# Optimization experiments

Measured on AMD Instinct MI355X. Metric: run time of the kernel, lower is better.

Reference implementation:

```python
import jax, jax.numpy as jnp
import numpy as np

N_NODES = 200000
N_EDGES = 440000
N_GRAPHS = 4096
EMB = 300
N_LAYERS = 5
TEMP = 0.04
NUM_ATOM_TYPE, NUM_CHIRALITY = 120, 3
NUM_BOND_TYPE, NUM_BOND_DIR = 6, 3
SELF_LOOP_TYPE = 4  # pretrain-gnns convention: self-loop edge_attr = [4, 0]


def setup_inputs() -> dict:
    key = jax.random.key(0)
    ks = jax.random.split(key, 24)
    inp = {}
    for i in (0, 1):
        inp[f"x{i}"] = jax.random.randint(ks[i * 4 + 0], (N_NODES, 2), 0, 3)
        inp[f"edge_index{i}"] = jax.random.randint(ks[i * 4 + 1], (2, N_EDGES), 0, N_NODES)
        inp[f"edge_attr{i}"] = jax.random.randint(ks[i * 4 + 2], (N_EDGES, 2), 0, 3)
        inp[f"batch_ids{i}"] = jnp.sort(jax.random.randint(ks[i * 4 + 3], (N_NODES,), 0, N_GRAPHS))

    def rn(k, shape, s=0.1):
        return (jax.random.normal(k, shape, jnp.float32) * s)

    inp["atom_emb1"] = rn(ks[8], (NUM_ATOM_TYPE, EMB))
    inp["atom_emb2"] = rn(ks[9], (NUM_CHIRALITY, EMB))
    inp["edge_emb1"] = rn(ks[10], (N_LAYERS, NUM_BOND_TYPE, EMB))
    inp["edge_emb2"] = rn(ks[11], (N_LAYERS, NUM_BOND_DIR, EMB))
    inp["W1"] = rn(ks[12], (N_LAYERS, EMB, 2 * EMB))
    inp["bm1"] = jnp.zeros((N_LAYERS, 2 * EMB), jnp.float32)
    inp["W2"] = rn(ks[13], (N_LAYERS, 2 * EMB, EMB))
    inp["bm2"] = jnp.zeros((N_LAYERS, EMB), jnp.float32)
    inp["gamma"] = jnp.ones((N_LAYERS, EMB), jnp.float32)
    inp["beta"] = jnp.zeros((N_LAYERS, EMB), jnp.float32)
    inp["Wp1"] = rn(ks[14], (EMB, EMB))
    inp["bp1"] = jnp.zeros((EMB,), jnp.float32)
    inp["Wp2"] = rn(ks[15], (EMB, EMB))
    inp["bp2"] = jnp.zeros((EMB,), jnp.float32)
    return inp


def _encode(x, edge_index, edge_attr, batch_ids,
            atom_emb1, atom_emb2, edge_emb1, edge_emb2,
            W1, bm1, W2, bm2, gamma, beta, Wp1, bp1, Wp2, bp2):
    n = x.shape[0]
    src, dst = edge_index[0], edge_index[1]
    h = atom_emb1[x[:, 0]] + atom_emb2[x[:, 1]]  # [N, EMB]
    for l in range(N_LAYERS):
        e = edge_emb1[l][edge_attr[:, 0]] + edge_emb2[l][edge_attr[:, 1]]  # [E, EMB]
        self_e = edge_emb1[l][SELF_LOOP_TYPE] + edge_emb2[l][0]  # self-loop edge emb
        # GIN sum aggregation (incl. self-loop message h_i + self_e)
        agg = jax.ops.segment_sum(h[src] + e, dst, num_segments=n) + h + self_e
        h = jax.nn.relu(agg @ W1[l] + bm1[l]) @ W2[l] + bm2[l]
        # BatchNorm over nodes (training-mode statistics, eps=1e-5)
        mean = h.mean(axis=0)
        var = h.var(axis=0)
        h = (h - mean) * jax.lax.rsqrt(var + 1e-5) * gamma[l] + beta[l]
        if l < N_LAYERS - 1:
            h = jax.nn.relu(h)
    # global_mean_pool
    s = jax.ops.segment_sum(h, batch_ids, num_segments=N_GRAPHS)
    c = jax.ops.segment_sum(jnp.ones((n, 1), h.dtype), batch_ids, num_segments=N_GRAPHS)
    g = s / jnp.maximum(c, 1.0)
    out = jax.nn.relu(g @ Wp1 + bp1) @ Wp2 + bp2
    return out / jnp.linalg.norm(out, axis=1, keepdims=True)


def reference(x0, edge_index0, edge_attr0, batch_ids0,
              x1, edge_index1, edge_attr1, batch_ids1,
              atom_emb1, atom_emb2, edge_emb1, edge_emb2,
              W1, bm1, W2, bm2, gamma, beta, Wp1, bp1, Wp2, bp2):
    params = (atom_emb1, atom_emb2, edge_emb1, edge_emb2,
              W1, bm1, W2, bm2, gamma, beta, Wp1, bp1, Wp2, bp2)
    f0 = _encode(x0, edge_index0, edge_attr0, batch_ids0, *params)
    f1 = _encode(x1, edge_index1, edge_attr1, batch_ids1, *params)
    logits = (f0 @ f1.T) / TEMP
    labels = jnp.arange(logits.shape[0])
    return logits, labels
```

## Files before the change

kernel.cpp:

```cpp
#include <hip/hip_runtime.h>
#include <hip/hip_bf16.h>
#include <hip/hip_fp16.h>

#define EMB 300
#define NHID 600
#define NLAYERS 5
#define NG 4096
#define NCOMBO 18
#define SELFCB 12
#define HS 304
#define KP1 320
#define KP2 640
#define SCB 2048

__device__ __forceinline__ void atomAddF(float* p, float v) { unsafeAtomicAdd(p, v); }

struct f8 { unsigned char v; };

__device__ __forceinline__ unsigned char enc8(float x) {
    unsigned xb = __float_as_uint(x);
    unsigned s = (xb >> 24) & 0x80u;
    float a = __uint_as_float(xb & 0x7FFFFFFFu);
    if (!(a < 448.f)) return (unsigned char)(s | 0x7E);
    if (a < 0.0009765625f) return (unsigned char)s;
    if (a < 0.015625f) {
        int m = (int)(a * 512.f + 0.5f);
        if (m > 7) return (unsigned char)(s | 0x08);
        return (unsigned char)(s | (unsigned)m);
    }
    unsigned u = __float_as_uint(a) + 0x80000u;
    int e = (int)(u >> 23) - 127;
    if (e > 8) return (unsigned char)(s | 0x7E);
    unsigned m = (u >> 20) & 7u;
    return (unsigned char)(s | ((unsigned)(e + 7) << 3) | m);
}
__device__ __forceinline__ float dec8(unsigned char c) {
    unsigned s = c & 0x80u, e = (c >> 3) & 0xFu, m = c & 7u;
    float v = (e == 0) ? (float)m * 0.001953125f
                       : __uint_as_float(((e + 120u) << 23) | (m << 20));
    return s ? -v : v;
}

typedef float fx2 __attribute__((ext_vector_type(2)));

#if defined(__has_builtin)
#if __has_builtin(__builtin_amdgcn_cvt_pk_f32_fp8) && __has_builtin(__builtin_amdgcn_cvt_pk_fp8_f32)
#define HWFP8 1
#endif
#endif

__device__ __forceinline__ void dec4(unsigned w, float& v0, float& v1, float& v2, float& v3) {
#ifdef HWFP8
    fx2 lo = __builtin_amdgcn_cvt_pk_f32_fp8((int)w, false);
    fx2 hi = __builtin_amdgcn_cvt_pk_f32_fp8((int)w, true);
    v0 = lo.x; v1 = lo.y; v2 = hi.x; v3 = hi.y;
#else
    v0 = dec8(w & 0xff); v1 = dec8((w >> 8) & 0xff);
    v2 = dec8((w >> 16) & 0xff); v3 = dec8((w >> 24) & 0xff);
#endif
}
__device__ __forceinline__ unsigned enc4(float v0, float v1, float v2, float v3) {
#ifdef HWFP8
    int w = __builtin_amdgcn_cvt_pk_fp8_f32(v0, v1, 0, false);
    w = __builtin_amdgcn_cvt_pk_fp8_f32(v2, v3, w, true);
    return (unsigned)w;
#else
    return (unsigned)enc8(v0) | ((unsigned)enc8(v1) << 8)
         | ((unsigned)enc8(v2) << 16) | ((unsigned)enc8(v3) << 24);
#endif
}
__device__ __forceinline__ unsigned char enc1(float v) {
#ifdef HWFP8
    return (unsigned char)(__builtin_amdgcn_cvt_pk_fp8_f32(v, 0.f, 0, false) & 0xff);
#else
    return enc8(v);
#endif
}
__device__ __forceinline__ float dec1(unsigned char c) {
#ifdef HWFP8
    fx2 lo = __builtin_amdgcn_cvt_pk_f32_fp8((int)(unsigned)c, false);
    return lo.x;
#else
    return dec8(c);
#endif
}

typedef _Float16 f16t;
typedef _Float16 f16x8 __attribute__((ext_vector_type(8)));
typedef float f32x4 __attribute__((ext_vector_type(4)));

__device__ __forceinline__ void stF(float* p, float v) { *p = v; }
__device__ __forceinline__ void stF(__half* p, float v) { *p = __float2half(v); }


__global__ void zero_f32_v6(float* __restrict__ p, long n) {
    long s = (long)gridDim.x * blockDim.x;
    for (long i = blockIdx.x * (long)blockDim.x + threadIdx.x; i < n; i += s) p[i] = 0.f;
}
__global__ void zero_i32_v8(int* __restrict__ p, int n) {
    int s = gridDim.x * blockDim.x;
    for (int i = blockIdx.x * blockDim.x + threadIdx.x; i < n; i += s) p[i] = 0;
}
__global__ void copy_i32_v8(const int* __restrict__ a, int* __restrict__ b, int n) {
    int s = gridDim.x * blockDim.x;
    for (int i = blockIdx.x * blockDim.x + threadIdx.x; i < n; i += s) b[i] = a[i];
}
__global__ void labels_v6(float* __restrict__ out, int n) {
    int i = blockIdx.x * blockDim.x + threadIdx.x;
    if (i < n) out[i] = (float)i;
}


__global__ void hist_dst_v8(const int* __restrict__ ei, int* __restrict__ deg, int E) {
    int s = gridDim.x * blockDim.x;
    for (int e = blockIdx.x * blockDim.x + threadIdx.x; e < E; e += s)
        atomicAdd(&deg[ei[E + e]], 1);
}
__global__ void hist_b_v8(const int* __restrict__ b, int* __restrict__ deg, int n) {
    int s = gridDim.x * blockDim.x;
    for (int i = blockIdx.x * blockDim.x + threadIdx.x; i < n; i += s)
        atomicAdd(&deg[b[i]], 1);
}

__global__ __launch_bounds__(256) void scan_excl_v8(const int* __restrict__ in,
                                                    int* __restrict__ out, int n) {
    __shared__ int part[256];
    int span = (n + 255) / 256;
    int t = threadIdx.x;
    int s0 = t * span, s1 = min(s0 + span, n);
    int sum = 0;
    for (int i = s0; i < s1; ++i) sum += in[i];
    part[t] = sum;
    __syncthreads();
    int v = sum;
    for (int off = 1; off < 256; off <<= 1) {
        int u = (t >= off) ? part[t - off] : 0;
        __syncthreads();
        part[t] += u;
        __syncthreads();
    }
    int run = part[t] - v;
    for (int i = s0; i < s1; ++i) { out[i] = run; run += in[i]; }
    if (t == 255) out[n] = run;
}

__global__ __launch_bounds__(256) void scan_bsum_v10(const int* __restrict__ in,
                                                     int* __restrict__ bsum, int n) {
    __shared__ int red[256];
    int b = blockIdx.x, t = threadIdx.x;
    int base = b * SCB + t * 8;
    int s = 0;
#pragma unroll
    for (int i = 0; i < 8; ++i) { int idx = base + i; if (idx < n) s += in[idx]; }
    red[t] = s; __syncthreads();
#pragma unroll
    for (int o = 128; o > 0; o >>= 1) {
        if (t < o) red[t] += red[t + o];
        __syncthreads();
    }
    if (t == 0) bsum[b] = red[0];
}

__global__ __launch_bounds__(256) void scan_top_v10(int* __restrict__ bsum, int nb,
                                                    int* __restrict__ total_out) {
    __shared__ int part[256];
    int t = threadIdx.x;
    int v = (t < nb) ? bsum[t] : 0;
    part[t] = v;
    __syncthreads();
    for (int o = 1; o < 256; o <<= 1) {
        int u = (t >= o) ? part[t - o] : 0;
        __syncthreads();
        part[t] += u;
        __syncthreads();
    }
    if (t < nb) bsum[t] = part[t] - v;
    if (t == 255) *total_out = part[255];
}

__global__ __launch_bounds__(256) void scan_fill_v10(const int* __restrict__ in,
                                                     const int* __restrict__ bsum,
                                                     int* __restrict__ out, int n) {
    __shared__ int red[256];
    int b = blockIdx.x, t = threadIdx.x;
    int base = b * SCB + t * 8;
    int v[8]; int s = 0;
#pragma unroll
    for (int i = 0; i < 8; ++i) { int idx = base + i; v[i] = (idx < n) ? in[idx] : 0; s += v[i]; }
    red[t] = s;
    __syncthreads();
    int self = s;
    for (int o = 1; o < 256; o <<= 1) {
        int u = (t >= o) ? red[t - o] : 0;
        __syncthreads();
        red[t] += u;
        __syncthreads();
    }
    int run = bsum[b] + red[t] - self;
#pragma unroll
    for (int i = 0; i < 8; ++i) { int idx = base + i; if (idx < n) out[idx] = run; run += v[i]; }
}

__global__ void fill_csr_v8(const int* __restrict__ ei, const int* __restrict__ ea,
                            int* __restrict__ cursor, int* __restrict__ csrc,
                            int* __restrict__ ccombo, int E) {
    int s = gridDim.x * blockDim.x;
    for (int e = blockIdx.x * blockDim.x + threadIdx.x; e < E; e += s) {
        int dst = ei[E + e];
        int pos = atomicAdd(&cursor[dst], 1);
        csrc[pos] = ei[e];
        ccombo[pos] = ea[2 * e] * 3 + ea[2 * e + 1];
    }
}

__global__ void tbl_v8(const float* __restrict__ ee1, const float* __restrict__ ee2,
                       float* __restrict__ tbl) {
    int idx = blockIdx.x * blockDim.x + threadIdx.x;
    if (idx >= NLAYERS * NCOMBO * EMB) return;
    int j = idx % EMB;
    int cb = (idx / EMB) % NCOMBO;
    int l = idx / (EMB * NCOMBO);
    tbl[idx] = ee1[(l * 6 + cb / 3) * EMB + j] + ee2[(l * 3 + cb % 3) * EMB + j];
}

__global__ void wtrans_v9(const float* __restrict__ W, f16t* __restrict__ Wt,
                          int K, int N, int Kpad) {
    int idx = blockIdx.x * blockDim.x + threadIdx.x;
    if (idx >= N * Kpad) return;
    int n = idx / Kpad, k = idx - n * Kpad;
    Wt[idx] = (k < K) ? (f16t)W[(size_t)k * N + n] : (f16t)0.f;
}

__global__ void wtrans8_v13(const float* __restrict__ W, unsigned char* __restrict__ Wt,
                            int K, int N, int Kpad) {
    int idx = blockIdx.x * blockDim.x + threadIdx.x;
    if (idx >= N * Kpad) return;
    int n = idx / Kpad, k = idx - n * Kpad;
    Wt[idx] = (k < K) ? enc8(W[(size_t)k * N + n]) : 0;
}


__global__ void init_h_v11(const int* __restrict__ x, const float* __restrict__ ae1,
                           const float* __restrict__ ae2, unsigned char* __restrict__ h,
                           int N) {
    int s = gridDim.x * blockDim.x;
    int total = N * (HS / 4);
    for (int idx = blockIdx.x * blockDim.x + threadIdx.x; idx < total; idx += s) {
        int i = idx / (HS / 4), d = idx - i * (HS / 4);
        int j = d * 4;
        int x0 = x[2 * i] * EMB, x1 = x[2 * i + 1] * EMB;
        unsigned out = 0;
#pragma unroll
        for (int t = 0; t < 4; ++t) {
            int jj = j + t;
            unsigned char b = 0;
            if (jj < EMB) b = enc8(ae1[x0 + jj] + ae2[x1 + jj]);
            out |= (unsigned)b << (8 * t);
        }
        *(unsigned*)(h + (size_t)i * HS + j) = out;
    }
}

template<bool BN>
__global__ __launch_bounds__(256)
void gather_v16(const unsigned char* __restrict__ h, const int* __restrict__ rp,
                const int* __restrict__ csrc, const int* __restrict__ ccombo,
                const float* __restrict__ tbl, const float* __restrict__ scl,
                const float* __restrict__ sft, unsigned char* __restrict__ aggc,
                int c0, int c1) {
    __shared__ float T[NCOMBO * EMB];
    __shared__ float SC[EMB + 4];
    __shared__ float SF[EMB + 4];
    for (int t = threadIdx.x; t < NCOMBO * EMB; t += 256) T[t] = tbl[t];
    if (BN) {
        for (int t = threadIdx.x; t < EMB; t += 256) { SC[t] = scl[t]; SF[t] = sft[t]; }
    }
    __syncthreads();
    int wid = (blockIdx.x * blockDim.x + threadIdx.x) >> 6;
    int lane = threadIdx.x & 63;
    int nw = (gridDim.x * blockDim.x) >> 6;
    const int jt = 256 + lane;
    float4 sc4, sf4; float sct = 1.f, sff = 0.f;
    if (BN) {
        sc4 = *(const float4*)&SC[lane << 2];
        sf4 = *(const float4*)&SF[lane << 2];
        if (lane < 44) { sct = SC[jt]; sff = SF[jt]; }
    }
#define BNAPP(val, sc, sf) { if (BN) (val) = fmaxf(fmaf((val), (sc), (sf)), 0.f); }
    for (int i = c0 + wid; i < c1; i += nw) {
        int p0 = rp[i], p1 = rp[i + 1];
        int src = (p0 < p1) ? csrc[p0] : 0;
        int cb  = (p0 < p1) ? ccombo[p0] : 0;
        float a0, a1, a2, a3, at = 0.f;
        {
            const unsigned char* hr = h + (size_t)i * HS;
            unsigned w = *(const unsigned*)(hr + (lane << 2));
            float4 t4 = *(const float4*)&T[SELFCB * EMB + (lane << 2)];
            float v0, v1, v2, v3;
            dec4(w, v0, v1, v2, v3);
            BNAPP(v0, sc4.x, sf4.x); BNAPP(v1, sc4.y, sf4.y);
            BNAPP(v2, sc4.z, sf4.z); BNAPP(v3, sc4.w, sf4.w);
            a0 = v0 + t4.x; a1 = v1 + t4.y; a2 = v2 + t4.z; a3 = v3 + t4.w;
            if (lane < 44) {
                float vt = dec1(hr[jt]);
                BNAPP(vt, sct, sff);
                at = vt + T[SELFCB * EMB + jt];
            }
        }
        for (int p = p0; p < p1; ++p) {
            int nsrc = 0, ncb = 0;
            if (p + 1 < p1) { nsrc = csrc[p + 1]; ncb = ccombo[p + 1]; }
            const unsigned char* hs = h + (size_t)src * HS;
            unsigned w = *(const unsigned*)(hs + (lane << 2));
            float4 t4 = *(const float4*)&T[cb * EMB + (lane << 2)];
            float v0, v1, v2, v3;
            dec4(w, v0, v1, v2, v3);
            BNAPP(v0, sc4.x, sf4.x); BNAPP(v1, sc4.y, sf4.y);
            BNAPP(v2, sc4.z, sf4.z); BNAPP(v3, sc4.w, sf4.w);
            a0 += v0 + t4.x; a1 += v1 + t4.y; a2 += v2 + t4.z; a3 += v3 + t4.w;
            if (lane < 44) {
                float vt = dec1(hs[jt]);
                BNAPP(vt, sct, sff);
                at += vt + T[cb * EMB + jt];
            }
            src = nsrc; cb = ncb;
        }
        unsigned char* out = aggc + (size_t)(i - c0) * KP1;
        *(unsigned*)(out + (lane << 2)) = enc4(a0, a1, a2, a3);
        if (lane < 44) out[jt] = enc1(at);
    }
#undef BNAPP
}

template<int MODE, bool STATS>
__global__ __launch_bounds__(256)
void fast_gemm8_v16(const unsigned char* __restrict__ A, int lda,
                    const unsigned char* __restrict__ Bt, int ldb,
                    const float* __restrict__ bias, unsigned char* __restrict__ C,
                    int ldc, int M, int N, int Kpad, int gx,
                    float* __restrict__ sums)
{
    __shared__ char smem[26624];
    char* AlB = smem;
    char* BlB = smem + 9216;
    const int tid = threadIdx.x;
    const int lane = tid & 63;
    const int wid = tid >> 6;
    const int wr = (wid >> 1) << 6;
    const int wc = (wid & 1) << 6;

    const int nwg = gridDim.x;
    const int q = nwg >> 3, r = nwg & 7;
    const int xcd = blockIdx.x & 7, idx = blockIdx.x >> 3;
    const int swz = (xcd < r ? xcd * (q + 1) : r * (q + 1) + (xcd - r) * q) + idx;
    const int row0 = (swz / gx) * 128;
    const int col0 = (swz % gx) * 128;

    f32x4 acc[4][4] = {};
    const int nkt = Kpad >> 6;
    const int sr = tid >> 1;
    const int skb = (tid & 1) << 5;

    for (int kt = 0; kt < nkt; ++kt) {
        const int k0 = kt << 6;
        {
            const int gr = row0 + sr;
            const unsigned char* src = A + (size_t)gr * lda + k0 + skb;
            int4 v0 = {0, 0, 0, 0}, v1 = {0, 0, 0, 0};
            if (gr < M) { v0 = *(const int4*)src; v1 = *(const int4*)(src + 16); }
            char* dst = AlB + sr * 72 + skb;
            *(long*)(dst)      = ((const long*)&v0)[0];
            *(long*)(dst + 8)  = ((const long*)&v0)[1];
            *(long*)(dst + 16) = ((const long*)&v1)[0];
            *(long*)(dst + 24) = ((const long*)&v1)[1];
        }
        {
            const int gc = col0 + sr;
            const unsigned char* src = Bt + (size_t)gc * ldb + k0 + skb;
            int4 v0 = {0, 0, 0, 0}, v1 = {0, 0, 0, 0};
            if (gc < N) { v0 = *(const int4*)src; v1 = *(const int4*)(src + 16); }
            char* dst = BlB + sr * 72 + skb;
            *(long*)(dst)      = ((const long*)&v0)[0];
            *(long*)(dst + 8)  = ((const long*)&v0)[1];
            *(long*)(dst + 16) = ((const long*)&v1)[0];
            *(long*)(dst + 24) = ((const long*)&v1)[1];
        }
        __syncthreads();
        const int fr = lane & 15;
        const int kbase = (lane >> 4) << 3;
#pragma unroll
        for (int ks = 0; ks < 2; ++ks) {
            const int kg = kbase + ks * 32;
            long af[4], bf[4];
#pragma unroll
            for (int mi = 0; mi < 4; ++mi)
                af[mi] = *(const long*)(AlB + (wr + mi * 16 + fr) * 72 + kg);
#pragma unroll
            for (int ni = 0; ni < 4; ++ni)
                bf[ni] = *(const long*)(BlB + (wc + ni * 16 + fr) * 72 + kg);
#pragma unroll
            for (int mi = 0; mi < 4; ++mi)
#pragma unroll
                for (int ni = 0; ni < 4; ++ni)
                    acc[mi][ni] = __builtin_amdgcn_mfma_f32_16x16x32_fp8_fp8(
                        af[mi], bf[ni], acc[mi][ni], 0, 0, 0);
        }
        __syncthreads();
    }
    char* Cl = smem;
    float* Sred = (float*)(smem + 18432);
    float* Qred = (float*)(smem + 22528);
    const int fr = lane & 15;
    const int rb = (lane >> 4) << 2;
    const int slot = ((wid >> 1) << 2) | (lane >> 4);
#pragma unroll
    for (int ni = 0; ni < 4; ++ni) {
        const int cb = wc + ni * 16 + fr;
        const int c = col0 + cb;
        const float bv = (c < N) ? bias[c] : 0.f;
        float lsum = 0.f, lsq = 0.f;
#pragma unroll
        for (int mi = 0; mi < 4; ++mi) {
#pragma unroll
            for (int i = 0; i < 4; ++i) {
                const int rloc = wr + mi * 16 + rb + i;
                float v = acc[mi][ni][i] + bv;
                if (MODE == 2) v = fmaxf(v, 0.f);
                Cl[rloc * 144 + cb] = (char)enc1(v);
                if (STATS && (row0 + rloc) < M && c < N) {
                    lsum += v; lsq = fmaf(v, v, lsq);
                }
            }
        }
        if (STATS) { Sred[cb * 8 + slot] = lsum; Qred[cb * 8 + slot] = lsq; }
    }
    __syncthreads();
    {
        const int rloc = tid >> 1;
        const int half = (tid & 1) << 6;
        const int grow = row0 + rloc;
        if (grow < M) {
            int cmax = ldc - col0; if (cmax > 128) cmax = 128;
            unsigned char* dst = C + (size_t)grow * ldc + col0;
            const char* srcl = Cl + rloc * 144 + half;
#pragma unroll
            for (int qi = 0; qi < 4; ++qi) {
                if (half + qi * 16 + 16 <= cmax)
                    *(int4*)(dst + half + qi * 16) = *(const int4*)(srcl + qi * 16);
            }
        }
    }
    if (STATS) {
        if (tid < 128) {
            const int c = col0 + tid;
            if (c < N) {
                float s = 0.f, qq = 0.f;
#pragma unroll
                for (int k = 0; k < 8; ++k) { s += Sred[tid * 8 + k]; qq += Qred[tid * 8 + k]; }
                atomAddF(&sums[c], s);
                atomAddF(&sums[EMB + c], qq);
            }
        }
    }
}

template<typename TO, int MODE>
__global__ __launch_bounds__(256)
void fast_gemm_v12(const f16t* __restrict__ A, int lda,
                   const f16t* __restrict__ Bt, int ldb,
                   const float* __restrict__ bias, TO* __restrict__ C, int ldc,
                   int M, int N, int Kpad, float scale)
{
    __shared__ f16t Al[128][76];
    __shared__ f16t Bl[128][76];
    const int tid = threadIdx.x;
    const int lane = tid & 63;
    const int wid = tid >> 6;
    const int wr = (wid >> 1) << 6;
    const int wc = (wid & 1) << 6;
    const int row0 = blockIdx.y * 128;
    const int col0 = blockIdx.x * 128;
    f32x4 acc[4][4] = {};
    const int nkt = Kpad >> 6;
    const int sr = tid >> 1;
    const int skb = (tid & 1) << 5;

    for (int kt = 0; kt < nkt; ++kt) {
        const int k0 = kt << 6;
        {
            const int gr = row0 + sr;
            const f16t* src = A + (size_t)gr * lda + k0 + skb;
            f16x8 v0 = {}, v1 = {}, v2 = {}, v3 = {};
            if (gr < M) {
                v0 = *(const f16x8*)(src);
                v1 = *(const f16x8*)(src + 8);
                v2 = *(const f16x8*)(src + 16);
                v3 = *(const f16x8*)(src + 24);
            }
            *(f16x8*)&Al[sr][skb]      = v0;
            *(f16x8*)&Al[sr][skb + 8]  = v1;
            *(f16x8*)&Al[sr][skb + 16] = v2;
            *(f16x8*)&Al[sr][skb + 24] = v3;
        }
        {
            const int gc = col0 + sr;
            const f16t* src = Bt + (size_t)gc * ldb + k0 + skb;
            f16x8 v0 = {}, v1 = {}, v2 = {}, v3 = {};
            if (gc < N) {
                v0 = *(const f16x8*)(src);
                v1 = *(const f16x8*)(src + 8);
                v2 = *(const f16x8*)(src + 16);
                v3 = *(const f16x8*)(src + 24);
            }
            *(f16x8*)&Bl[sr][skb]      = v0;
            *(f16x8*)&Bl[sr][skb + 8]  = v1;
            *(f16x8*)&Bl[sr][skb + 16] = v2;
            *(f16x8*)&Bl[sr][skb + 24] = v3;
        }
        __syncthreads();
        const int fr = lane & 15;
        const int kbase = (lane >> 4) << 3;
#pragma unroll
        for (int ks = 0; ks < 2; ++ks) {
            const int kg8 = kbase + ks * 32;
            f16x8 af[4], bf[4];
#pragma unroll
            for (int mi = 0; mi < 4; ++mi)
                af[mi] = *(const f16x8*)&Al[wr + mi * 16 + fr][kg8];
#pragma unroll
            for (int ni = 0; ni < 4; ++ni)
                bf[ni] = *(const f16x8*)&Bl[wc + ni * 16 + fr][kg8];
#pragma unroll
            for (int mi = 0; mi < 4; ++mi)
#pragma unroll
                for (int ni = 0; ni < 4; ++ni)
                    acc[mi][ni] = __builtin_amdgcn_mfma_f32_16x16x32_f16(
                        af[mi], bf[ni], acc[mi][ni], 0, 0, 0);
        }
        __syncthreads();
    }
    const int fr = lane & 15;
    const int rb = (lane >> 4) << 2;
#pragma unroll
    for (int ni = 0; ni < 4; ++ni) {
        const int c = col0 + wc + ni * 16 + fr;
        if (c >= N) continue;
        const float bv = (MODE == 1 || MODE == 2) ? bias[c] : 0.f;
#pragma unroll
        for (int mi = 0; mi < 4; ++mi) {
#pragma unroll
            for (int i = 0; i < 4; ++i) {
                const int r = row0 + wr + mi * 16 + rb + i;
                if (r >= M) continue;
                float v = acc[mi][ni][i];
                if (MODE == 1 || MODE == 2) v += bv;
                if (MODE == 2) v = fmaxf(v, 0.f);
                v *= scale;
                if (MODE == 3) v = fmaxf(-26.f, fminf(26.f, v));
                stF(&C[(size_t)r * ldc + c], v);
            }
        }
    }
}


__global__ void bn_finalize_v6(const float* __restrict__ sums,
                               const float* __restrict__ gamma, const float* __restrict__ beta,
                               float* __restrict__ scl, float* __restrict__ sft, float inv_n) {
    int j = threadIdx.x;
    if (j < EMB) {
        float m = sums[j] * inv_n;
        float var = sums[EMB + j] * inv_n - m * m;
        float sc = gamma[j] * rsqrtf(var + 1e-5f);
        scl[j] = sc;
        sft[j] = beta[j] - m * sc;
    }
}


__global__ __launch_bounds__(256) void pool_seg_v11(const unsigned char* __restrict__ h,
                                                    const int* __restrict__ gptr,
                                                    const float* __restrict__ scl,
                                                    const float* __restrict__ sft,
                                                    __half* __restrict__ poolh) {
    int g = blockIdx.x;
    int s0 = gptr[g], s1 = gptr[g + 1];
    float inv = (s1 > s0) ? 1.f / (float)(s1 - s0) : 0.f;
    for (int j = threadIdx.x; j < EMB; j += 256) {
        float s = 0.f;
        for (int r = s0; r < s1; ++r) s += dec1(h[(size_t)r * HS + j]);
        float mv = (s1 > s0) ? fmaf(s * inv, scl[j], sft[j]) : 0.f;
        poolh[(size_t)g * KP1 + j] = __float2half(mv);
    }
}


__global__ __launch_bounds__(256) void rownorm_f16_v12(const float* __restrict__ f,
                                                       f16t* __restrict__ fh) {
    __shared__ float red[256];
    __shared__ float inv;
    int r = blockIdx.x, tid = threadIdx.x;
    const float* row = f + (size_t)r * EMB;
    float s = 0.f;
    for (int j = tid; j < EMB; j += 256) { float v = row[j]; s = fmaf(v, v, s); }
    red[tid] = s;
    __syncthreads();
#pragma unroll
    for (int o = 128; o > 0; o >>= 1) {
        if (tid < o) red[tid] += red[tid + o];
        __syncthreads();
    }
    if (tid == 0) inv = rsqrtf(fmaxf(red[0], 1e-30f));
    __syncthreads();
    float iv = inv;
    for (int j = tid; j < KP1; j += 256)
        fh[(size_t)r * KP1 + j] = (j < EMB) ? (f16t)(row[j] * iv) : (f16t)0.f;
}


extern "C" void kernel_launch(void* const* d_in, const int* in_sizes, int n_in,
                              void* d_out, int out_size, void* d_ws, size_t ws_size,
                              hipStream_t stream) {
    const int N = in_sizes[0] / 2;
    const int E = in_sizes[1] / 2;

    const float* atom1 = (const float*)d_in[8];
    const float* atom2 = (const float*)d_in[9];
    const float* ee1   = (const float*)d_in[10];
    const float* ee2   = (const float*)d_in[11];
    const float* W1    = (const float*)d_in[12];
    const float* bm1   = (const float*)d_in[13];
    const float* W2    = (const float*)d_in[14];
    const float* bm2   = (const float*)d_in[15];
    const float* gamma = (const float*)d_in[16];
    const float* beta  = (const float*)d_in[17];
    const float* Wp1   = (const float*)d_in[18];
    const float* bp1   = (const float*)d_in[19];
    const float* Wp2   = (const float*)d_in[20];
    const float* bp2   = (const float*)d_in[21];

    float* ob = (float*)d_out;

    unsigned char* h0 = (unsigned char*)d_out;
    bool h0_fits = ((size_t)N * HS) <= ((size_t)NG * NG * 4 - 256);

    size_t off = 0;
    char* base = (char*)d_ws;
    auto take = [&](size_t bytes) -> char* {
        char* p = base + off;
        off += (bytes + 255) & ~(size_t)255;
        return p;
    };
    unsigned char* h1 = (unsigned char*)take((size_t)N * HS);
    float* fbuf   = (float*)take((size_t)NG * EMB * 4);
    f16t*  fh     = (f16t*)take((size_t)2 * NG * KP1 * 2);
    float* sums   = (float*)take(2 * EMB * 4);
    float* scl    = (float*)take((size_t)NLAYERS * EMB * 4);
    float* sft    = (float*)take((size_t)NLAYERS * EMB * 4);
    int*   deg    = (int*)take((size_t)N * 4);
    int*   rp     = (int*)take((size_t)(N + 1) * 4);
    int*   cursor = (int*)take((size_t)N * 4);
    int*   csrc   = (int*)take((size_t)E * 4);
    int*   ccombo = (int*)take((size_t)E * 4);
    int*   bsum   = (int*)take(256 * 4);
    int*   gdeg   = (int*)take((size_t)NG * 4);
    int*   gptr   = (int*)take((size_t)(NG + 1) * 4);
    float* tbl    = (float*)take((size_t)NLAYERS * NCOMBO * EMB * 4);
    unsigned char* W1t8 = (unsigned char*)take((size_t)NLAYERS * NHID * KP1);
    unsigned char* W2t8 = (unsigned char*)take((size_t)NLAYERS * EMB * KP2);
    f16t*  Wp1t   = (f16t*)take((size_t)EMB * KP1 * 2);
    f16t*  Wp2t   = (f16t*)take((size_t)EMB * KP1 * 2);
    __half* poolh = (__half*)take((size_t)NG * KP1 * 2);
    __half* p1h   = (__half*)take((size_t)NG * KP1 * 2);

    long CN = 0;
    if (h0_fits && ws_size > off + 1024) {
        CN = (long)((ws_size - off - 1024) / (KP1 + KP2));
        if (CN > N) CN = N;
    }
    if (CN < 1024) {
        zero_f32_v6<<<2048, 256, 0, stream>>>(ob, (long)NG * NG);
        labels_v6<<<(NG + 255) / 256, 256, 0, stream>>>(ob + (size_t)NG * NG, NG);
        return;
    }
    unsigned char* aggc = (unsigned char*)take((size_t)CN * KP1);
    unsigned char* z    = (unsigned char*)take((size_t)CN * KP2);

    tbl_v8<<<(NLAYERS * NCOMBO * EMB + 255) / 256, 256, 0, stream>>>(ee1, ee2, tbl);
    for (int l = 0; l < NLAYERS; ++l) {
        wtrans8_v13<<<(NHID * KP1 + 255) / 256, 256, 0, stream>>>(
            W1 + (size_t)l * EMB * NHID, W1t8 + (size_t)l * NHID * KP1, EMB, NHID, KP1);
        wtrans8_v13<<<(EMB * KP2 + 255) / 256, 256, 0, stream>>>(
            W2 + (size_t)l * NHID * EMB, W2t8 + (size_t)l * EMB * KP2, NHID, EMB, KP2);
    }
    wtrans_v9<<<(EMB * KP1 + 255) / 256, 256, 0, stream>>>(Wp1, Wp1t, EMB, EMB, KP1);
    wtrans_v9<<<(EMB * KP1 + 255) / 256, 256, 0, stream>>>(Wp2, Wp2t, EMB, EMB, KP1);
    zero_f32_v6<<<2048, 256, 0, stream>>>((float*)aggc, CN * (KP1 / 4));
    zero_f32_v6<<<2048, 256, 0, stream>>>((float*)z, CN * (KP2 / 4));
    zero_f32_v6<<<1024, 256, 0, stream>>>((float*)poolh, (long)NG * (KP1 / 2));
    zero_f32_v6<<<1024, 256, 0, stream>>>((float*)p1h, (long)NG * (KP1 / 2));

    const int nb = (N + SCB - 1) / SCB;

    for (int enc = 0; enc < 2; ++enc) {
        const int* x  = (const int*)d_in[enc * 4 + 0];
        const int* ei = (const int*)d_in[enc * 4 + 1];
        const int* ea = (const int*)d_in[enc * 4 + 2];
        const int* bi = (const int*)d_in[enc * 4 + 3];

        zero_i32_v8<<<256, 256, 0, stream>>>(deg, N);
        hist_dst_v8<<<1024, 256, 0, stream>>>(ei, deg, E);
        scan_bsum_v10<<<nb, 256, 0, stream>>>(deg, bsum, N);
        scan_top_v10<<<1, 256, 0, stream>>>(bsum, nb, rp + N);
        scan_fill_v10<<<nb, 256, 0, stream>>>(deg, bsum, rp, N);
        copy_i32_v8<<<256, 256, 0, stream>>>(rp, cursor, N);
        fill_csr_v8<<<1024, 256, 0, stream>>>(ei, ea, cursor, csrc, ccombo, E);
        zero_i32_v8<<<64, 256, 0, stream>>>(gdeg, NG);
        hist_b_v8<<<1024, 256, 0, stream>>>(bi, gdeg, N);
        scan_excl_v8<<<1, 256, 0, stream>>>(gdeg, gptr, NG);

        unsigned char* hc = h0;
        unsigned char* hn = h1;
        init_h_v11<<<4096, 256, 0, stream>>>(x, atom1, atom2, hc, N);

        for (int l = 0; l < NLAYERS; ++l) {
            const unsigned char* W1l = W1t8 + (size_t)l * NHID * KP1;
            const unsigned char* W2l = W2t8 + (size_t)l * EMB * KP2;
            const float* tl = tbl + (size_t)l * NCOMBO * EMB;
            const float* scp = scl + (size_t)(l - 1) * EMB;
            const float* sfp = sft + (size_t)(l - 1) * EMB;

            zero_f32_v6<<<1, 1024, 0, stream>>>(sums, 2 * EMB);

            for (long c0 = 0; c0 < N; c0 += CN) {
                int m = (int)((N - c0 < CN) ? (N - c0) : CN);
                if (l == 0)
                    gather_v16<false><<<2048, 256, 0, stream>>>(
                        hc, rp, csrc, ccombo, tl, nullptr, nullptr,
                        aggc, (int)c0, (int)(c0 + m));
                else
                    gather_v16<true><<<2048, 256, 0, stream>>>(
                        hc, rp, csrc, ccombo, tl, scp, sfp,
                        aggc, (int)c0, (int)(c0 + m));
                int gx1 = (NHID + 127) / 128, gy1 = (m + 127) / 128;
                fast_gemm8_v16<2, false><<<gx1 * gy1, 256, 0, stream>>>(
                    aggc, KP1, W1l, KP1, bm1 + l * NHID,
                    z, KP2, m, NHID, KP1, gx1, nullptr);
                int gx2 = (EMB + 127) / 128;
                fast_gemm8_v16<1, true><<<gx2 * gy1, 256, 0, stream>>>(
                    z, KP2, W2l, KP2, bm2 + l * EMB,
                    hn + (size_t)c0 * HS, HS, m, EMB, KP2, gx2, sums);
            }

            bn_finalize_v6<<<1, 320, 0, stream>>>(sums, gamma + l * EMB, beta + l * EMB,
                                                  scl + (size_t)l * EMB,
                                                  sft + (size_t)l * EMB, 1.f / (float)N);
            unsigned char* t = hc; hc = hn; hn = t;
        }

        pool_seg_v11<<<NG, 256, 0, stream>>>(hc, gptr,
                                             scl + (size_t)(NLAYERS - 1) * EMB,
                                             sft + (size_t)(NLAYERS - 1) * EMB, poolh);

        dim3 gp((EMB + 127) / 128, (NG + 127) / 128);
        fast_gemm_v12<__half, 2><<<gp, 256, 0, stream>>>(
            (const f16t*)poolh, KP1, Wp1t, KP1, bp1, p1h, KP1, NG, EMB, KP1, 1.f);
        fast_gemm_v12<float, 1><<<gp, 256, 0, stream>>>(
            (const f16t*)p1h, KP1, Wp2t, KP1, bp2, fbuf, EMB, NG, EMB, KP1, 1.f);
        rownorm_f16_v12<<<NG, 256, 0, stream>>>(fbuf, fh + (size_t)enc * NG * KP1);
    }

    f16t* f0h = fh;
    f16t* f1h = fh + (size_t)NG * KP1;
    dim3 gl(NG / 128, NG / 128);
    fast_gemm_v12<float, 3><<<gl, 256, 0, stream>>>(
        f0h, KP1, f1h, KP1, nullptr, ob, NG, NG, NG, KP1, 25.f);
    labels_v6<<<(NG + 255) / 256, 256, 0, stream>>>(ob + (size_t)NG * NG, NG);
}
```

Before: 4.374 ms.

## Double-buffer LDS tiles in FP8 GEMM with register prefetch of next K tile

The FP8 MFMA GEMM now prefetches the next K-tile from global memory into registers while computing on the current LDS buffer, then writes it into a second LDS buffer. This removes one barrier per iteration and is meant to hide global load latency behind the MFMA work. The LDS row stride also changes from 72 to 76 bytes, which alters the bank mapping, and total LDS grows to about 39KB. That may reduce occupancy, and the epilogue still uses fixed offsets that must fit inside the larger buffer.

```diff
diff --git a/kernel.cpp b/kernel.cpp
--- a/kernel.cpp
+++ b/kernel.cpp
@@ -12,6 +12,7 @@
 #define KP1 320
 #define KP2 640
 #define SCB 2048
+#define LSTR 76
 
 __device__ __forceinline__ void atomAddF(float* p, float v) { unsafeAtomicAdd(p, v); }
 
@@ -334,15 +335,13 @@
 
 template<int MODE, bool STATS>
 __global__ __launch_bounds__(256)
-void fast_gemm8_v16(const unsigned char* __restrict__ A, int lda,
+void fast_gemm8_v17(const unsigned char* __restrict__ A, int lda,
                     const unsigned char* __restrict__ Bt, int ldb,
                     const float* __restrict__ bias, unsigned char* __restrict__ C,
                     int ldc, int M, int N, int Kpad, int gx,
                     float* __restrict__ sums)
 {
-    __shared__ char smem[26624];
-    char* AlB = smem;
-    char* BlB = smem + 9216;
+    __shared__ char smem[4 * 128 * LSTR];
     const int tid = threadIdx.x;
     const int lane = tid & 63;
     const int wid = tid >> 6;
@@ -360,53 +359,77 @@
     const int nkt = Kpad >> 6;
     const int sr = tid >> 1;
     const int skb = (tid & 1) << 5;
-
+    const int gr = row0 + sr;
+    const int gc = col0 + sr;
+    const unsigned char* Abase = A + (size_t)gr * lda + skb;
+    const unsigned char* Bbase = Bt + (size_t)gc * ldb + skb;
+
+    int4 av0 = {0,0,0,0}, av1 = {0,0,0,0}, bv0 = {0,0,0,0}, bv1 = {0,0,0,0};
+    if (gr < M) { av0 = *(const int4*)(Abase); av1 = *(const int4*)(Abase + 16); }
+    if (gc < N) { bv0 = *(const int4*)(Bbase); bv1 = *(const int4*)(Bbase + 16); }
+    {
+        char* da = smem + sr * LSTR + skb;
+        *(long*)(da)      = ((const long*)&av0)[0];
+        *(long*)(da + 8)  = ((const long*)&av0)[1];
+        *(long*)(da + 16) = ((const long*)&av1)[0];
+        *(long*)(da + 24) = ((const long*)&av1)[1];
+        char* db = smem + 128 * LSTR + sr * LSTR + skb;
+        *(long*)(db)      = ((const long*)&bv0)[0];
+        *(long*)(db + 8)  = ((const long*)&bv0)[1];
+        *(long*)(db + 16) = ((const long*)&bv1)[0];
+        *(long*)(db + 24) = ((const long*)&bv1)[1];
+    }
+    __syncthreads();
+
+    int cur = 0;
     for (int kt = 0; kt < nkt; ++kt) {
-        const int k0 = kt << 6;
+        const bool more = (kt + 1) < nkt;
+        if (more) {
+            const int kn = (kt + 1) << 6;
+            av0 = {0,0,0,0}; av1 = {0,0,0,0}; bv0 = {0,0,0,0}; bv1 = {0,0,0,0};
+            if (gr < M) { av0 = *(const int4*)(Abase + kn); av1 = *(const int4*)(Abase + kn + 16); }
+            if (gc < N) { bv0 = *(const int4*)(Bbase + kn); bv1 = *(const int4*)(Bbase + kn + 16); }
+        }
         {
-            const int gr = row0 + sr;
-            const unsigned char* src = A + (size_t)gr * lda + k0 + skb;
-            int4 v0 = {0, 0, 0, 0}, v1 = {0, 0, 0, 0};
-            if (gr < M) { v0 = *(const int4*)src; v1 = *(const int4*)(src + 16); }
-            char* dst = AlB + sr * 72 + skb;
-            *(long*)(dst)      = ((const long*)&v0)[0];
-            *(long*)(dst + 8)  = ((const long*)&v0)[1];
-            *(long*)(dst + 16) = ((const long*)&v1)[0];
-            *(long*)(dst + 24) = ((const long*)&v1)[1];
-        }
-        {
-            const int gc = col0 + sr;
-            const unsigned char* src = Bt + (size_t)gc * ldb + k0 + skb;
-            int4 v0 = {0, 0, 0, 0}, v1 = {0, 0, 0, 0};
-            if (gc < N) { v0 = *(const int4*)src; v1 = *(const int4*)(src + 16); }
-            char* dst = BlB + sr * 72 + skb;
-            *(long*)(dst)      = ((const long*)&v0)[0];
-            *(long*)(dst + 8)  = ((const long*)&v0)[1];
-            *(long*)(dst + 16) = ((const long*)&v1)[0];
-            *(long*)(dst + 24) = ((const long*)&v1)[1];
-        }
-        __syncthreads();
-        const int fr = lane & 15;
-        const int kbase = (lane >> 4) << 3;
-#pragma unroll
-        for (int ks = 0; ks < 2; ++ks) {
-            const int kg = kbase + ks * 32;
-            long af[4], bf[4];
-#pragma unroll
-            for (int mi = 0; mi < 4; ++mi)
-                af[mi] = *(const long*)(AlB + (wr + mi * 16 + fr) * 72 + kg);
-#pragma unroll
-            for (int ni = 0; ni < 4; ++ni)
-                bf[ni] = *(const long*)(BlB + (wc + ni * 16 + fr) * 72 + kg);
-#pragma unroll
-            for (int mi = 0; mi < 4; ++mi)
+            const char* AlB = smem + (cur ? 2 * 128 * LSTR : 0);
+            const char* BlB = AlB + 128 * LSTR;
+            const int fr = lane & 15;
+            const int kbase = (lane >> 4) << 3;
+#pragma unroll
+            for (int ks = 0; ks < 2; ++ks) {
+                const int kg = kbase + ks * 32;
+                long af[4], bf[4];
+#pragma unroll
+                for (int mi = 0; mi < 4; ++mi)
+                    af[mi] = *(const long*)(AlB + (wr + mi * 16 + fr) * LSTR + kg);
 #pragma unroll
                 for (int ni = 0; ni < 4; ++ni)
-                    acc[mi][ni] = __builtin_amdgcn_mfma_f32_16x16x32_fp8_fp8(
-                        af[mi], bf[ni], acc[mi][ni], 0, 0, 0);
-        }
-        __syncthreads();
-    }
+                    bf[ni] = *(const long*)(BlB + (wc + ni * 16 + fr) * LSTR + kg);
+#pragma unroll
+                for (int mi = 0; mi < 4; ++mi)
+#pragma unroll
+                    for (int ni = 0; ni < 4; ++ni)
+                        acc[mi][ni] = __builtin_amdgcn_mfma_f32_16x16x32_fp8_fp8(
+                            af[mi], bf[ni], acc[mi][ni], 0, 0, 0);
+            }
+        }
+        if (more) {
+            char* base2 = smem + (cur ? 0 : 2 * 128 * LSTR);
+            char* da = base2 + sr * LSTR + skb;
+            *(long*)(da)      = ((const long*)&av0)[0];
+            *(long*)(da + 8)  = ((const long*)&av0)[1];
+            *(long*)(da + 16) = ((const long*)&av1)[0];
+            *(long*)(da + 24) = ((const long*)&av1)[1];
+            char* db = base2 + 128 * LSTR + sr * LSTR + skb;
+            *(long*)(db)      = ((const long*)&bv0)[0];
+            *(long*)(db + 8)  = ((const long*)&bv0)[1];
+            *(long*)(db + 16) = ((const long*)&bv1)[0];
+            *(long*)(db + 24) = ((const long*)&bv1)[1];
+        }
+        __syncthreads();
+        cur ^= 1;
+    }
+
     char* Cl = smem;
     float* Sred = (float*)(smem + 18432);
     float* Qred = (float*)(smem + 22528);
@@ -743,11 +766,11 @@
                         hc, rp, csrc, ccombo, tl, scp, sfp,
                         aggc, (int)c0, (int)(c0 + m));
                 int gx1 = (NHID + 127) / 128, gy1 = (m + 127) / 128;
-                fast_gemm8_v16<2, false><<<gx1 * gy1, 256, 0, stream>>>(
+                fast_gemm8_v17<2, false><<<gx1 * gy1, 256, 0, stream>>>(
                     aggc, KP1, W1l, KP1, bm1 + l * NHID,
                     z, KP2, m, NHID, KP1, gx1, nullptr);
                 int gx2 = (EMB + 127) / 128;
-                fast_gemm8_v16<1, true><<<gx2 * gy1, 256, 0, stream>>>(
+                fast_gemm8_v17<1, true><<<gx2 * gy1, 256, 0, stream>>>(
                     z, KP2, W2l, KP2, bm2 + l * EMB,
                     hn + (size_t)c0 * HS, HS, m, EMB, KP2, gx2, sums);
             }
```

Result: slower. 11.54 ms (+163.9%).
